# Kernel optimization log

Measured on AMD Instinct MI355X. Metric: run time of the kernel, lower is better.

Reference implementation:

```python
import jax, jax.numpy as jnp
import numpy as np

N = 100000   # total nodes in batched graph
E = 600000   # total edges
B = 64       # graphs in batch
H = 128      # hidden_dim
A = 64       # action_dim
L = 4        # num mpnn layers
LOG_STD_MIN, LOG_STD_MAX = -20.0, 2.0


def setup_inputs() -> dict:
    key = jax.random.key(0)
    ks = jax.random.split(key, 40)
    s = 0.05

    def w(k, shape):
        return (jax.random.normal(k, shape, jnp.float32) * s)

    inp = {}
    inp["node_feat"] = jax.random.normal(ks[0], (N, 7), jnp.float32)
    inp["edge_feat"] = jax.random.normal(ks[1], (E, 2), jnp.float32)
    # node encoder: Linear(7,H) -> ReLU -> Linear(H,H)
    inp["ne_w1"] = w(ks[2], (7, H)); inp["ne_b1"] = jnp.zeros((H,), jnp.float32)
    inp["ne_w2"] = w(ks[3], (H, H)); inp["ne_b2"] = jnp.zeros((H,), jnp.float32)
    # edge encoder: Linear(2,H) -> ReLU -> Linear(H,H)
    inp["ee_w1"] = w(ks[4], (2, H)); inp["ee_b1"] = jnp.zeros((H,), jnp.float32)
    inp["ee_w2"] = w(ks[5], (H, H)); inp["ee_b2"] = jnp.zeros((H,), jnp.float32)
    # per-layer message net: Linear(3H,H) -> ReLU -> Linear(H,H)  (stacked over L)
    inp["msg_w1"] = w(ks[6], (L, 3 * H, H)); inp["msg_b1"] = jnp.zeros((L, H), jnp.float32)
    inp["msg_w2"] = w(ks[7], (L, H, H));     inp["msg_b2"] = jnp.zeros((L, H), jnp.float32)
    # per-layer update net: Linear(2H,H) -> ReLU -> Linear(H,H)
    inp["upd_w1"] = w(ks[8], (L, 2 * H, H)); inp["upd_b1"] = jnp.zeros((L, H), jnp.float32)
    inp["upd_w2"] = w(ks[9], (L, H, H));     inp["upd_b2"] = jnp.zeros((L, H), jnp.float32)
    # attention-pooling gate: Linear(H,H) -> ReLU -> Linear(H,1)
    inp["gate_w1"] = w(ks[10], (H, H)); inp["gate_b1"] = jnp.zeros((H,), jnp.float32)
    inp["gate_w2"] = w(ks[11], (H, 1)); inp["gate_b2"] = jnp.zeros((1,), jnp.float32)
    # policy net: Linear(H,H) -> ReLU -> Linear(H,H) -> ReLU -> Linear(H,2A)
    inp["pol_w1"] = w(ks[12], (H, H));     inp["pol_b1"] = jnp.zeros((H,), jnp.float32)
    inp["pol_w2"] = w(ks[13], (H, H));     inp["pol_b2"] = jnp.zeros((H,), jnp.float32)
    inp["pol_w3"] = w(ks[14], (H, 2 * A)); inp["pol_b3"] = jnp.zeros((2 * A,), jnp.float32)
    # graph connectivity
    inp["src"] = jax.random.randint(ks[15], (E,), 0, N)
    inp["dst"] = jax.random.randint(ks[16], (E,), 0, N)
    inp["graph_id"] = jnp.sort(jax.random.randint(ks[17], (N,), 0, B))
    return inp


def _mlp2(x, w1, b1, w2, b2):
    return jax.nn.relu(x @ w1 + b1) @ w2 + b2


def reference(node_feat, edge_feat,
              ne_w1, ne_b1, ne_w2, ne_b2,
              ee_w1, ee_b1, ee_w2, ee_b2,
              msg_w1, msg_b1, msg_w2, msg_b2,
              upd_w1, upd_b1, upd_w2, upd_b2,
              gate_w1, gate_b1, gate_w2, gate_b2,
              pol_w1, pol_b1, pol_w2, pol_b2, pol_w3, pol_b3,
              src, dst, graph_id):
    # encode
    h = _mlp2(node_feat, ne_w1, ne_b1, ne_w2, ne_b2)          # [N, H]
    e = _mlp2(edge_feat, ee_w1, ee_b1, ee_w2, ee_b2)          # [E, H]
    # MPNN layers with residual (h = layer(h) + h)
    for l in range(L):
        msg_in = jnp.concatenate([h[src], h[dst], e], axis=1)  # [E, 3H]
        m = _mlp2(msg_in, msg_w1[l], msg_b1[l], msg_w2[l], msg_b2[l])  # [E, H]
        h_agg = jax.ops.segment_sum(m, dst, num_segments=N)    # [N, H]
        upd_in = jnp.concatenate([h, h_agg], axis=1)           # [N, 2H]
        h = _mlp2(upd_in, upd_w1[l], upd_b1[l], upd_w2[l], upd_b2[l]) + h
    # global attention pooling (per-graph segment softmax over gate logits)
    gate = _mlp2(h, gate_w1, gate_b1, gate_w2, gate_b2)[:, 0]  # [N]
    gmax = jax.ops.segment_max(gate, graph_id, num_segments=B)  # [B]
    ex = jnp.exp(gate - gmax[graph_id])                        # [N]
    z = jax.ops.segment_sum(ex, graph_id, num_segments=B)      # [B]
    alpha = ex / z[graph_id]                                   # [N]
    emb = jax.ops.segment_sum(alpha[:, None] * h, graph_id, num_segments=B)  # [B, H]
    # policy head
    out = jax.nn.relu(jax.nn.relu(emb @ pol_w1 + pol_b1) @ pol_w2 + pol_b2) @ pol_w3 + pol_b3  # [B, 2A]
    mean, log_std = out[:, :A], out[:, A:]
    log_std = jnp.clip(log_std, LOG_STD_MIN, LOG_STD_MAX)
    std = jnp.exp(log_std)
    return (mean, std)
```

## Files before the change

kernel.cpp:

```cpp
#include <hip/hip_runtime.h>
#include <stdint.h>

#define NN 100000
#define NE 600000
#define NG 64
#define HD 128
#define HD2 (HD*HD)
#define NLAYER 4
#define SCAN_NB 391
#define NTILES ((NN + 63) / 64)
#define PSLICE 16

typedef unsigned short u16;
typedef unsigned int u32;
typedef unsigned long long u64;
typedef __attribute__((ext_vector_type(8))) short bf16x8;
typedef __attribute__((ext_vector_type(4))) float f32x4;

__device__ __forceinline__ float bf2f(u32 v) { return __uint_as_float(v << 16); }
__device__ __forceinline__ u16 f2bf(float f) {
    u32 u = __float_as_uint(f);
    return (u16)((u + 0x7FFFu + ((u >> 16) & 1u)) >> 16);
}
__device__ __forceinline__ u32 pk2(float a, float b) {
    return (u32)f2bf(a) | ((u32)f2bf(b) << 16);
}

template<bool RELU, bool GATE>
__global__ __launch_bounds__(256, 3) void mgemm_kernel(
    const u16* __restrict__ Xb, const u16* __restrict__ Wt,
    const float* __restrict__ bias, const float* __restrict__ degscale,
    const u16* __restrict__ addend, u16* __restrict__ out, int M,
    const float* __restrict__ gw2, const float* __restrict__ gb2,
    float* __restrict__ gate)
{
    __shared__ u16 WsL[HD * HD];
    __shared__ u16 XsL[64 * HD];
    const int t = threadIdx.x;
    const int lane = t & 63, wave = t >> 6;
    const int cj = ((lane >> 4) << 2);

    for (int i = t; i < HD * 16; i += 256) {
        const int row = i >> 4, c16 = i & 15;
        uint4 v = *(const uint4*)(Wt + (size_t)row * HD + c16 * 8);
        *(uint4*)((char*)WsL + (((row << 8) + (c16 << 4)) ^ ((row & 7) << 4))) = v;
    }
    float4 bcol[8];
    #pragma unroll
    for (int ct = 0; ct < 8; ct++)
        bcol[ct] = bias ? *(const float4*)(bias + ct * 16 + cj)
                        : make_float4(0.f, 0.f, 0.f, 0.f);
    float4 gwv[8];
    if (GATE) {
        #pragma unroll
        for (int ct = 0; ct < 8; ct++)
            gwv[ct] = *(const float4*)(gw2 + ct * 16 + cj);
    }

    const int arow = wave * 16 + (lane & 15);
    const int alin = (arow << 8) + ((lane >> 4) << 4);
    const int axor = (arow & 7) << 4;
    __syncthreads();

    for (int tile = blockIdx.x; tile < NTILES; tile += gridDim.x) {
        const int r0 = tile << 6;
        for (int i = t; i < 64 * 16; i += 256) {
            const int row = i >> 4, c16 = i & 15;
            const int rg = r0 + row;
            uint4 v = make_uint4(0, 0, 0, 0);
            if (rg < M) v = *(const uint4*)(Xb + (size_t)rg * HD + c16 * 8);
            *(uint4*)((char*)XsL + (((row << 8) + (c16 << 4)) ^ ((row & 7) << 4))) = v;
        }
        __syncthreads();

        bf16x8 a[4];
        #pragma unroll
        for (int ks = 0; ks < 4; ks++)
            a[ks] = *(const bf16x8*)((const char*)XsL + ((alin + ks * 64) ^ axor));

        f32x4 acc[8];
        #pragma unroll
        for (int ct = 0; ct < 8; ct++) {
            acc[ct][0] = 0.f; acc[ct][1] = 0.f; acc[ct][2] = 0.f; acc[ct][3] = 0.f;
        }
        #pragma unroll
        for (int ct = 0; ct < 8; ct++) {
            const int bn = ct * 16 + (lane & 15);
            #pragma unroll
            for (int ks = 0; ks < 4; ks++) {
                bf16x8 breg = *(const bf16x8*)((const char*)WsL +
                    (((bn << 8) + ks * 64 + ((lane >> 4) << 4)) ^ ((bn & 7) << 4)));
                acc[ct] = __builtin_amdgcn_mfma_f32_16x16x32_bf16(breg, a[ks], acc[ct], 0, 0, 0);
            }
        }

        const int orow = r0 + wave * 16 + (lane & 15);
        const bool rv = orow < M;
        float gdot = 0.f;
        const float ds = (degscale && rv) ? degscale[orow] : 1.f;
        #pragma unroll
        for (int ct = 0; ct < 8; ct++) {
            const int c0 = ct * 16 + cj;
            float v0 = acc[ct][0], v1 = acc[ct][1], v2 = acc[ct][2], v3 = acc[ct][3];
            if (bias) {
                v0 += bcol[ct].x * ds; v1 += bcol[ct].y * ds;
                v2 += bcol[ct].z * ds; v3 += bcol[ct].w * ds;
            }
            if (addend && rv) {
                ushort4 av = *(const ushort4*)(addend + (size_t)orow * HD + c0);
                v0 += bf2f(av.x); v1 += bf2f(av.y); v2 += bf2f(av.z); v3 += bf2f(av.w);
            }
            if (RELU) {
                v0 = fmaxf(v0, 0.f); v1 = fmaxf(v1, 0.f);
                v2 = fmaxf(v2, 0.f); v3 = fmaxf(v3, 0.f);
            }
            if (GATE) {
                gdot += v0 * gwv[ct].x + v1 * gwv[ct].y + v2 * gwv[ct].z + v3 * gwv[ct].w;
            } else if (rv) {
                ushort4 pk;
                pk.x = f2bf(v0); pk.y = f2bf(v1); pk.z = f2bf(v2); pk.w = f2bf(v3);
                *(ushort4*)(out + (size_t)orow * HD + c0) = pk;
            }
        }
        if (GATE) {
            gdot += __shfl_xor(gdot, 16, 64);
            gdot += __shfl_xor(gdot, 32, 64);
            if ((lane >> 4) == 0 && rv) gate[orow] = gdot + gb2[0];
        }
        __syncthreads();
    }
}

__global__ __launch_bounds__(256, 2) void pqgemm_kernel(
    const u16* __restrict__ Xb, const u16* __restrict__ WtP,
    const u16* __restrict__ WtQ, u16* __restrict__ outP,
    u16* __restrict__ outQ, int M)
{
    __shared__ u16 WsL[2 * HD * HD];
    __shared__ u16 XsL[64 * HD];
    const int t = threadIdx.x;
    const int lane = t & 63, wave = t >> 6;
    const int cj = ((lane >> 4) << 2);

    for (int i = t; i < 2 * HD * 16; i += 256) {
        const int w = i >> 11;
        const int j = i & 2047;
        const int row = j >> 4, c16 = j & 15;
        const u16* Wt = w ? WtQ : WtP;
        uint4 v = *(const uint4*)(Wt + (size_t)row * HD + c16 * 8);
        *(uint4*)((char*)WsL + w * 32768 +
                  (((row << 8) + (c16 << 4)) ^ ((row & 7) << 4))) = v;
    }

    const int arow = wave * 16 + (lane & 15);
    const int alin = (arow << 8) + ((lane >> 4) << 4);
    const int axor = (arow & 7) << 4;
    __syncthreads();

    for (int tile = blockIdx.x; tile < NTILES; tile += gridDim.x) {
        const int r0 = tile << 6;
        for (int i = t; i < 64 * 16; i += 256) {
            const int row = i >> 4, c16 = i & 15;
            const int rg = r0 + row;
            uint4 v = make_uint4(0, 0, 0, 0);
            if (rg < M) v = *(const uint4*)(Xb + (size_t)rg * HD + c16 * 8);
            *(uint4*)((char*)XsL + (((row << 8) + (c16 << 4)) ^ ((row & 7) << 4))) = v;
        }
        __syncthreads();

        bf16x8 a[4];
        #pragma unroll
        for (int ks = 0; ks < 4; ks++)
            a[ks] = *(const bf16x8*)((const char*)XsL + ((alin + ks * 64) ^ axor));

        const int orow = r0 + wave * 16 + (lane & 15);
        const bool rv = orow < M;

        #pragma unroll
        for (int o = 0; o < 2; o++) {
            f32x4 acc[8];
            #pragma unroll
            for (int ct = 0; ct < 8; ct++) {
                acc[ct][0] = 0.f; acc[ct][1] = 0.f; acc[ct][2] = 0.f; acc[ct][3] = 0.f;
            }
            #pragma unroll
            for (int ct = 0; ct < 8; ct++) {
                const int bn = ct * 16 + (lane & 15);
                #pragma unroll
                for (int ks = 0; ks < 4; ks++) {
                    bf16x8 breg = *(const bf16x8*)((const char*)WsL + o * 32768 +
                        (((bn << 8) + ks * 64 + ((lane >> 4) << 4)) ^ ((bn & 7) << 4)));
                    acc[ct] = __builtin_amdgcn_mfma_f32_16x16x32_bf16(breg, a[ks], acc[ct], 0, 0, 0);
                }
            }
            if (rv) {
                u16* out = o ? outQ : outP;
                #pragma unroll
                for (int ct = 0; ct < 8; ct++) {
                    ushort4 pk;
                    pk.x = f2bf(acc[ct][0]); pk.y = f2bf(acc[ct][1]);
                    pk.z = f2bf(acc[ct][2]); pk.w = f2bf(acc[ct][3]);
                    *(ushort4*)(out + (size_t)orow * HD + ct * 16 + cj) = pk;
                }
            }
        }
        __syncthreads();
    }
}

__global__ __launch_bounds__(256, 2) void edge_mfma_kernel(
    const float2* __restrict__ sef, const int* __restrict__ ssrc,
    const int* __restrict__ sdst, const int* __restrict__ off,
    const float* __restrict__ ew1, const float* __restrict__ eb1,
    const u16* __restrict__ Mt, const float* __restrict__ mvec,
    const u16* __restrict__ P, const u16* __restrict__ Q,
    u16* __restrict__ agg)
{
    __shared__ __align__(16) char XHT[HD * 72 * 2];
    __shared__ u16 PsL[64 * 136];
    __shared__ u16 QsL[32 * 136];
    __shared__ u64 dlocL[8];
    __shared__ float ew1L[2 * HD];
    __shared__ float eb1L[HD];
    u16* HT = (u16*)XHT;
    const int t = threadIdx.x, lane = t & 63, wave = t >> 6;
    const int cj = (lane >> 4) << 2;
    const int n0 = blockIdx.x * 32;

    ew1L[t] = ew1[t];
    if (t < HD) eb1L[t] = eb1[t];
    for (int i = t; i < 32 * 32; i += 256) {
        const int row = i >> 5, c4 = (i & 31) * 4;
        *(ushort4*)(QsL + row * 136 + c4) = *(const ushort4*)(Q + (size_t)(n0 + row) * HD + c4);
    }

    float4 mvv[8];
    #pragma unroll
    for (int ct = 0; ct < 8; ct++) mvv[ct] = *(const float4*)(mvec + ct * 16 + cj);

    bf16x8 breg[8][4];
    #pragma unroll
    for (int ct = 0; ct < 8; ct++) {
        const int bn = ct * 16 + (lane & 15);
        #pragma unroll
        for (int ks = 0; ks < 4; ks++)
            breg[ct][ks] = *(const bf16x8*)(Mt + (size_t)bn * HD + ks * 32 + ((lane >> 4) << 3));
    }

    const int rt = wave & 1;
    const int c2b = (wave >> 1) * 4;
    const int nodeid = rt * 16 + (lane & 15);
    f32x4 acc2[4];
    #pragma unroll
    for (int i = 0; i < 4; i++) {
        acc2[i][0] = 0.f; acc2[i][1] = 0.f; acc2[i][2] = 0.f; acc2[i][3] = 0.f;
    }

    const int e0 = off[n0], e1 = off[n0 + 32];
    const int arow = wave * 16 + (lane & 15);
    const int alin = (arow << 8) + ((lane >> 4) << 4);
    const int axor = (arow & 7) << 4;
    const int el = wave * 16 + (lane & 15);
    __syncthreads();

    for (int base = e0; base < e1; base += 64) {
        for (int i = t; i < 64 * 16; i += 256) {
            const int row = i >> 4, c16 = i & 15;
            const int e = base + row;
            uint4 v = make_uint4(0, 0, 0, 0);
            uint4 pvv = make_uint4(0, 0, 0, 0);
            if (e < e1) {
                const float2 f = sef[e];
                const int c8 = c16 * 8;
                float o[8];
                #pragma unroll
                for (int k = 0; k < 8; k++)
                    o[k] = fmaxf(f.x * ew1L[c8 + k] + f.y * ew1L[HD + c8 + k] + eb1L[c8 + k], 0.f);
                v = make_uint4(pk2(o[0], o[1]), pk2(o[2], o[3]), pk2(o[4], o[5]), pk2(o[6], o[7]));
                const int srcI = ssrc[e];
                pvv = *(const uint4*)(P + (size_t)srcI * HD + c16 * 8);
            }
            *(uint4*)(XHT + (((row << 8) + (c16 << 4)) ^ ((row & 7) << 4))) = v;
            *(uint4*)(PsL + row * 136 + c16 * 8) = pvv;
        }
        if (t < 64) {
            const int e = base + t;
            ((unsigned char*)dlocL)[t] = (e < e1) ? (unsigned char)(sdst[e] - n0) : (unsigned char)0xFF;
        }
        __syncthreads();

        bf16x8 a[4];
        #pragma unroll
        for (int ks = 0; ks < 4; ks++)
            a[ks] = *(const bf16x8*)(XHT + ((alin + ks * 64) ^ axor));
        const int e = base + el;
        const bool ev = e < e1;
        const int dl = ev ? (int)((const unsigned char*)dlocL)[el] : 0;
        __syncthreads();

        f32x4 acc[8];
        #pragma unroll
        for (int ct = 0; ct < 8; ct++) {
            acc[ct][0] = 0.f; acc[ct][1] = 0.f; acc[ct][2] = 0.f; acc[ct][3] = 0.f;
        }
        #pragma unroll
        for (int ct = 0; ct < 8; ct++)
            #pragma unroll
            for (int ks = 0; ks < 4; ks++)
                acc[ct] = __builtin_amdgcn_mfma_f32_16x16x32_bf16(breg[ct][ks], a[ks], acc[ct], 0, 0, 0);

        #pragma unroll
        for (int ct = 0; ct < 8; ct++) {
            float v0 = 0.f, v1 = 0.f, v2 = 0.f, v3 = 0.f;
            if (ev) {
                const ushort4 pvc = *(const ushort4*)(PsL + el * 136 + ct * 16 + cj);
                const ushort4 qvc = *(const ushort4*)(QsL + dl * 136 + ct * 16 + cj);
                v0 = fmaxf(acc[ct][0] + bf2f(pvc.x) + bf2f(qvc.x) + mvv[ct].x, 0.f);
                v1 = fmaxf(acc[ct][1] + bf2f(pvc.y) + bf2f(qvc.y) + mvv[ct].y, 0.f);
                v2 = fmaxf(acc[ct][2] + bf2f(pvc.z) + bf2f(qvc.z) + mvv[ct].z, 0.f);
                v3 = fmaxf(acc[ct][3] + bf2f(pvc.w) + bf2f(qvc.w) + mvv[ct].w, 0.f);
            }
            const int c0 = ct * 16 + cj;
            HT[(c0 + 0) * 72 + el] = f2bf(v0);
            HT[(c0 + 1) * 72 + el] = f2bf(v1);
            HT[(c0 + 2) * 72 + el] = f2bf(v2);
            HT[(c0 + 3) * 72 + el] = f2bf(v3);
        }
        __syncthreads();

        #pragma unroll
        for (int ks2 = 0; ks2 < 2; ks2++) {
            const u64 dv = dlocL[ks2 * 4 + (lane >> 4)];
            bf16x8 sfrag;
            #pragma unroll
            for (int j = 0; j < 8; j++) {
                const int dvj = (int)((dv >> (8 * j)) & 0xFF);
                sfrag[j] = (dvj == nodeid) ? (short)0x3F80 : (short)0;
            }
            #pragma unroll
            for (int i = 0; i < 4; i++) {
                const int col = (c2b + i) * 16 + (lane & 15);
                bf16x8 hfrag = *(const bf16x8*)(HT + col * 72 + ks2 * 32 + ((lane >> 4) << 3));
                acc2[i] = __builtin_amdgcn_mfma_f32_16x16x32_bf16(sfrag, hfrag, acc2[i], 0, 0, 0);
            }
        }
        __syncthreads();
    }

    u16* BNC = (u16*)XHT;
    #pragma unroll
    for (int i = 0; i < 4; i++) {
        const int col = (c2b + i) * 16 + (lane & 15);
        #pragma unroll
        for (int r = 0; r < 4; r++) {
            const int nl = rt * 16 + ((lane >> 4) << 2) + r;
            BNC[nl * 136 + col] = f2bf(acc2[i][r]);
        }
    }
    __syncthreads();
    for (int i = t; i < 32 * 16; i += 256) {
        const int row = i >> 4, c16 = i & 15;
        *(uint4*)(agg + (size_t)(n0 + row) * HD + c16 * 8) =
            *(const uint4*)(BNC + row * 136 + c16 * 8);
    }
}

__global__ __launch_bounds__(256) void gemm128_kernel(
    const float* __restrict__ X, const float* __restrict__ W,
    float* __restrict__ out, int M)
{
    __shared__ float Ws[HD * HD];
    __shared__ float Xs[32 * HD];
    const int t = threadIdx.x;
    for (int i = t; i < HD * HD / 4; i += 256)
        ((float4*)Ws)[i] = ((const float4*)W)[i];
    const int c0 = (t & 31) * 4;
    const int rb = (t >> 5) * 4;
    __syncthreads();
    const int ntiles = M / 32;
    for (int tile = blockIdx.x; tile < ntiles; tile += gridDim.x) {
        const int r0 = tile * 32;
        const float4* xg = (const float4*)(X + (size_t)r0 * HD);
        for (int i = t; i < 32 * HD / 4; i += 256)
            ((float4*)Xs)[i] = xg[i];
        __syncthreads();
        float acc[4][4];
        #pragma unroll
        for (int a = 0; a < 4; a++)
            #pragma unroll
            for (int b = 0; b < 4; b++) acc[a][b] = 0.f;
        for (int k = 0; k < HD; k += 4) {
            float4 w0 = *(const float4*)(Ws + (k + 0) * HD + c0);
            float4 w1 = *(const float4*)(Ws + (k + 1) * HD + c0);
            float4 w2 = *(const float4*)(Ws + (k + 2) * HD + c0);
            float4 w3 = *(const float4*)(Ws + (k + 3) * HD + c0);
            #pragma unroll
            for (int rr = 0; rr < 4; rr++) {
                float4 xv = *(const float4*)(Xs + (rb + rr) * HD + k);
                acc[rr][0] += xv.x * w0.x + xv.y * w1.x + xv.z * w2.x + xv.w * w3.x;
                acc[rr][1] += xv.x * w0.y + xv.y * w1.y + xv.z * w2.y + xv.w * w3.y;
                acc[rr][2] += xv.x * w0.z + xv.y * w1.z + xv.z * w2.z + xv.w * w3.z;
                acc[rr][3] += xv.x * w0.w + xv.y * w1.w + xv.z * w2.w + xv.w * w3.w;
            }
        }
        #pragma unroll
        for (int rr = 0; rr < 4; rr++) {
            const int row = r0 + rb + rr;
            *(float4*)(out + (size_t)row * HD + c0) =
                make_float4(acc[rr][0], acc[rr][1], acc[rr][2], acc[rr][3]);
        }
        __syncthreads();
    }
}

__global__ void mvec_kernel(const float* __restrict__ vec,
                            const float* __restrict__ W,
                            const float* __restrict__ mb1,
                            float* __restrict__ out) {
    const int j = threadIdx.x;
    if (j < HD) {
        float s = mb1 ? mb1[j] : 0.f;
        for (int i = 0; i < HD; i++) s += vec[i] * W[(size_t)i * HD + j];
        out[j] = s;
    }
}

__global__ __launch_bounds__(256) void wprep_kernel(
    const float* __restrict__ msg_w1, const float* __restrict__ Mw2,
    const float* __restrict__ upd_w1, const float* __restrict__ upd_w2,
    const float* __restrict__ gw1, const float* __restrict__ ne_w2,
    const float* __restrict__ Mw, u16* __restrict__ wt)
{
    __shared__ float tileL[HD * (HD + 1)];
    const int b = blockIdx.x, t = threadIdx.x;
    const int l = b & 3;
    const float* S;
    if (b < 4)       S = msg_w1 + (size_t)l * 3 * HD2;
    else if (b < 8)  S = msg_w1 + (size_t)l * 3 * HD2 + HD2;
    else if (b < 12) S = Mw + (size_t)l * HD2;
    else if (b < 16) S = Mw2 + (size_t)l * HD2;
    else if (b < 20) S = upd_w1 + (size_t)l * 2 * HD2;
    else if (b < 24) S = upd_w1 + (size_t)l * 2 * HD2 + HD2;
    else if (b < 28) S = upd_w2 + (size_t)l * HD2;
    else if (b == 28) S = gw1;
    else             S = ne_w2;
    u16* D = wt + (size_t)b * HD2;
    for (int i = t; i < HD2; i += 256) {
        const int k = i >> 7, n = i & 127;
        tileL[k * (HD + 1) + n] = S[i];
    }
    __syncthreads();
    for (int i = t; i < HD2; i += 256) {
        const int n = i >> 7, k = i & 127;
        D[i] = f2bf(tileL[k * (HD + 1) + n]);
    }
}

__global__ __launch_bounds__(256) void ne1_kernel(
    const float* __restrict__ nf, const float* __restrict__ w1,
    const float* __restrict__ b1, u16* __restrict__ out)
{
    __shared__ float w1s[7 * HD];
    __shared__ float b1s[HD];
    const int t = threadIdx.x;
    for (int i = t; i < 7 * HD; i += 256) w1s[i] = w1[i];
    if (t < HD) b1s[t] = b1[t];
    __syncthreads();
    const int row = blockIdx.x * 32 + (t >> 3);
    const int c0 = (t & 7) * 16;
    if (row < NN) {
        float f[7];
        #pragma unroll
        for (int k = 0; k < 7; k++) f[k] = nf[(size_t)row * 7 + k];
        float o[16];
        #pragma unroll
        for (int c = 0; c < 16; c++) {
            float a = b1s[c0 + c];
            #pragma unroll
            for (int k = 0; k < 7; k++) a += f[k] * w1s[k * HD + c0 + c];
            o[c] = fmaxf(a, 0.f);
        }
        uint4 v0 = make_uint4(pk2(o[0], o[1]), pk2(o[2], o[3]), pk2(o[4], o[5]), pk2(o[6], o[7]));
        uint4 v1 = make_uint4(pk2(o[8], o[9]), pk2(o[10], o[11]), pk2(o[12], o[13]), pk2(o[14], o[15]));
        *(uint4*)(out + (size_t)row * HD + c0) = v0;
        *(uint4*)(out + (size_t)row * HD + c0 + 8) = v1;
    }
}

__global__ void deg_count_kernel(const int* __restrict__ dst, int* __restrict__ deg) {
    const int i = blockIdx.x * 256 + threadIdx.x;
    if (i < NE) atomicAdd(&deg[dst[i]], 1);
}
__global__ void scan1_kernel(const int* __restrict__ deg, int* __restrict__ part) {
    __shared__ int s[256];
    const int t = threadIdx.x, i = blockIdx.x * 256 + t;
    s[t] = (i < NN) ? deg[i] : 0;
    __syncthreads();
    for (int d = 128; d > 0; d >>= 1) { if (t < d) s[t] += s[t + d]; __syncthreads(); }
    if (t == 0) part[blockIdx.x] = s[0];
}
__global__ void scan2_kernel(int* __restrict__ part, int nb) {
    if (threadIdx.x == 0 && blockIdx.x == 0) {
        int run = 0;
        for (int b = 0; b < nb; b++) { const int v = part[b]; part[b] = run; run += v; }
    }
}
__global__ void scan3_kernel(const int* __restrict__ deg, const int* __restrict__ part,
                             int* __restrict__ off, int* __restrict__ pos) {
    __shared__ int s[256];
    const int t = threadIdx.x, i = blockIdx.x * 256 + t;
    const int v = (i < NN) ? deg[i] : 0;
    s[t] = v;
    __syncthreads();
    for (int d = 1; d < 256; d <<= 1) {
        const int x = (t >= d) ? s[t - d] : 0;
        __syncthreads();
        s[t] += x;
        __syncthreads();
    }
    const int excl = s[t] - v + part[blockIdx.x];
    if (i < NN) {
        off[i] = excl; pos[i] = excl;
        if (i == NN - 1) off[NN] = excl + v;
    }
}
__global__ void scatter_kernel(const int* __restrict__ src, const int* __restrict__ dst,
                               const float* __restrict__ ef, int* __restrict__ pos,
                               float2* __restrict__ sef, int* __restrict__ ssrc,
                               int* __restrict__ sdst) {
    const int e = blockIdx.x * 256 + threadIdx.x;
    if (e < NE) {
        const int d = dst[e];
        const int p = atomicAdd(&pos[d], 1);
        sef[p] = make_float2(ef[2 * e], ef[2 * e + 1]);
        ssrc[p] = src[e]; sdst[p] = d;
    }
}
__global__ void degf_kernel(const int* __restrict__ off, float* __restrict__ degf) {
    const int n = blockIdx.x * 256 + threadIdx.x;
    if (n < NN) degf[n] = (float)(off[n + 1] - off[n]);
}

__global__ void bounds_kernel(const int* __restrict__ gid, int* __restrict__ gs) {
    const int g = threadIdx.x;
    if (g <= NG) {
        int lo = 0, hi = NN;
        while (lo < hi) {
            const int mid = (lo + hi) >> 1;
            if (gid[mid] < g) lo = mid + 1; else hi = mid;
        }
        gs[g] = lo;
    }
}

__global__ __launch_bounds__(256) void poolA_kernel(
    const float* __restrict__ gate, const int* __restrict__ gs,
    float* __restrict__ ex, float* __restrict__ gz)
{
    __shared__ float red[256];
    const int g = blockIdx.x, t = threadIdx.x;
    const int s = gs[g], e = gs[g + 1];
    if (s >= e) {
        if (t == 0) gz[g] = 1.f;
        return;
    }
    float m = -3.4e38f;
    for (int i = s + t; i < e; i += 256) m = fmaxf(m, gate[i]);
    red[t] = m; __syncthreads();
    for (int d = 128; d > 0; d >>= 1) {
        if (t < d) red[t] = fmaxf(red[t], red[t + d]);
        __syncthreads();
    }
    const float gm = red[0];
    __syncthreads();
    float zs = 0.f;
    for (int i = s + t; i < e; i += 256) {
        const float ev = expf(gate[i] - gm);
        ex[i] = ev; zs += ev;
    }
    red[t] = zs; __syncthreads();
    for (int d = 128; d > 0; d >>= 1) {
        if (t < d) red[t] += red[t + d];
        __syncthreads();
    }
    if (t == 0) gz[g] = red[0];
}

__global__ __launch_bounds__(256) void poolB_kernel(
    const float* __restrict__ ex, const int* __restrict__ gs,
    const u16* __restrict__ hb, float* __restrict__ partial)
{
    __shared__ float redL[16][132];
    const int b = blockIdx.x;
    const int g = b / PSLICE, sl = b % PSLICE;
    const int lo = gs[g], hi = gs[g + 1];
    const int len = hi - lo;
    const int chunk = (len + PSLICE - 1) / PSLICE;
    const int ns = lo + sl * chunk;
    const int ne = min(ns + chunk, hi);
    const int t = threadIdx.x;
    const int c8 = (t & 15) * 8;
    const int ro = t >> 4;
    float acc[8] = {0.f, 0.f, 0.f, 0.f, 0.f, 0.f, 0.f, 0.f};
    for (int n = ns + ro; n < ne; n += 16) {
        const float w = ex[n];
        const ushort4 h0 = *(const ushort4*)(hb + (size_t)n * HD + c8);
        const ushort4 h1 = *(const ushort4*)(hb + (size_t)n * HD + c8 + 4);
        acc[0] += w * bf2f(h0.x); acc[1] += w * bf2f(h0.y);
        acc[2] += w * bf2f(h0.z); acc[3] += w * bf2f(h0.w);
        acc[4] += w * bf2f(h1.x); acc[5] += w * bf2f(h1.y);
        acc[6] += w * bf2f(h1.z); acc[7] += w * bf2f(h1.w);
    }
    #pragma unroll
    for (int j = 0; j < 8; j++) redL[ro][c8 + j] = acc[j];
    __syncthreads();
    if (t < HD) {
        float s = 0.f;
        #pragma unroll
        for (int r = 0; r < 16; r++) s += redL[r][t];
        partial[(size_t)b * HD + t] = s;
    }
}

__global__ void poolC_kernel(const float* __restrict__ partial,
                             const float* __restrict__ gz,
                             float* __restrict__ emb)
{
    const int g = blockIdx.x, t = threadIdx.x;
    float s = 0.f;
    #pragma unroll
    for (int sl = 0; sl < PSLICE; sl++)
        s += partial[(size_t)(g * PSLICE + sl) * HD + t];
    emb[(size_t)g * HD + t] = s / gz[g];
}

__global__ __launch_bounds__(256) void policy_kernel(
    const float* __restrict__ emb,
    const float* __restrict__ w1, const float* __restrict__ b1,
    const float* __restrict__ w2, const float* __restrict__ b2,
    const float* __restrict__ w3, const float* __restrict__ b3,
    float* __restrict__ out)
{
    __shared__ float A[NG * HD];
    __shared__ float Bs[NG * HD];
    const int t = threadIdx.x;
    for (int i = t; i < NG * HD / 4; i += 256)
        ((float4*)A)[i] = ((const float4*)emb)[i];
    __syncthreads();
    const int c0 = (t & 31) * 4;
    const int rb = (t >> 5) * 8;
    {
        float4 bv = *(const float4*)(b1 + c0);
        for (int rr = 0; rr < 8; rr++) {
            const int r = rb + rr;
            float a0 = bv.x, a1 = bv.y, a2 = bv.z, a3 = bv.w;
            for (int k = 0; k < HD; k++) {
                const float x = A[r * HD + k];
                float4 wv = *(const float4*)(w1 + k * HD + c0);
                a0 += x * wv.x; a1 += x * wv.y; a2 += x * wv.z; a3 += x * wv.w;
            }
            *(float4*)(Bs + r * HD + c0) =
                make_float4(fmaxf(a0, 0.f), fmaxf(a1, 0.f), fmaxf(a2, 0.f), fmaxf(a3, 0.f));
        }
    }
    __syncthreads();
    {
        float4 bv = *(const float4*)(b2 + c0);
        for (int rr = 0; rr < 8; rr++) {
            const int r = rb + rr;
            float a0 = bv.x, a1 = bv.y, a2 = bv.z, a3 = bv.w;
            for (int k = 0; k < HD; k++) {
                const float x = Bs[r * HD + k];
                float4 wv = *(const float4*)(w2 + k * HD + c0);
                a0 += x * wv.x; a1 += x * wv.y; a2 += x * wv.z; a3 += x * wv.w;
            }
            *(float4*)(A + r * HD + c0) =
                make_float4(fmaxf(a0, 0.f), fmaxf(a1, 0.f), fmaxf(a2, 0.f), fmaxf(a3, 0.f));
        }
    }
    __syncthreads();
    {
        float4 bv = *(const float4*)(b3 + c0);
        for (int rr = 0; rr < 8; rr++) {
            const int r = rb + rr;
            float a[4] = {bv.x, bv.y, bv.z, bv.w};
            for (int k = 0; k < HD; k++) {
                const float x = A[r * HD + k];
                float4 wv = *(const float4*)(w3 + k * HD + c0);
                a[0] += x * wv.x; a[1] += x * wv.y; a[2] += x * wv.z; a[3] += x * wv.w;
            }
            #pragma unroll
            for (int j = 0; j < 4; j++) {
                const int c = c0 + j;
                if (c < 64) {
                    out[r * 64 + c] = a[j];
                } else {
                    const float ls = fminf(fmaxf(a[j], -20.f), 2.f);
                    out[4096 + r * 64 + (c - 64)] = expf(ls);
                }
            }
        }
    }
}

extern "C" void kernel_launch(void* const* d_in, const int* in_sizes, int n_in,
                              void* d_out, int out_size, void* d_ws, size_t ws_size,
                              hipStream_t stream) {
    const float* node_feat = (const float*)d_in[0];
    const float* edge_feat = (const float*)d_in[1];
    const float* ne_w1 = (const float*)d_in[2];
    const float* ne_b1 = (const float*)d_in[3];
    const float* ne_w2 = (const float*)d_in[4];
    const float* ne_b2 = (const float*)d_in[5];
    const float* ee_w1 = (const float*)d_in[6];
    const float* ee_b1 = (const float*)d_in[7];
    const float* ee_w2 = (const float*)d_in[8];
    const float* ee_b2 = (const float*)d_in[9];
    const float* msg_w1 = (const float*)d_in[10];
    const float* msg_b1 = (const float*)d_in[11];
    const float* msg_w2 = (const float*)d_in[12];
    const float* msg_b2 = (const float*)d_in[13];
    const float* upd_w1 = (const float*)d_in[14];
    const float* upd_b1 = (const float*)d_in[15];
    const float* upd_w2 = (const float*)d_in[16];
    const float* upd_b2 = (const float*)d_in[17];
    const float* gate_w1 = (const float*)d_in[18];
    const float* gate_b1 = (const float*)d_in[19];
    const float* gate_w2 = (const float*)d_in[20];
    const float* gate_b2 = (const float*)d_in[21];
    const float* pol_w1 = (const float*)d_in[22];
    const float* pol_b1 = (const float*)d_in[23];
    const float* pol_w2 = (const float*)d_in[24];
    const float* pol_b2 = (const float*)d_in[25];
    const float* pol_w3 = (const float*)d_in[26];
    const float* pol_b3 = (const float*)d_in[27];
    const int* src = (const int*)d_in[28];
    const int* dst = (const int*)d_in[29];
    const int* gid = (const int*)d_in[30];

    char* p = (char*)d_ws;
    u16* hb   = (u16*)p;    p += (size_t)NN * HD * 2;
    u16* Pb   = (u16*)p;    p += (size_t)NN * HD * 2;
    u16* Qb   = (u16*)p;    p += (size_t)NN * HD * 2;
    u16* aggb = (u16*)p;    p += (size_t)NN * HD * 2;
    float2* sef = (float2*)p; p += (size_t)NE * 8;
    int* ssrc = (int*)p;    p += (size_t)NE * 4;
    int* sdst = (int*)p;    p += (size_t)NE * 4;
    int* off  = (int*)p;    p += (size_t)(NN + 4) * 4;
    int* pos  = (int*)p;    p += (size_t)NN * 4;
    int* deg  = (int*)p;    p += (size_t)NN * 4;
    float* degf = (float*)p; p += (size_t)NN * 4;
    float* gate = (float*)p; p += (size_t)NN * 4;
    float* ex   = (float*)p; p += (size_t)NN * 4;
    int* part = (int*)p;    p += 2048;
    int* gs   = (int*)p;    p += 512;
    float* gz   = (float*)p; p += 256;
    float* emb = (float*)p; p += (size_t)NG * HD * 4;
    float* partialP = (float*)p; p += (size_t)NG * PSLICE * HD * 4;
    float* Mw  = (float*)p; p += (size_t)NLAYER * HD2 * 4;
    float* Mw2 = (float*)p; p += (size_t)NLAYER * HD2 * 4;
    float* mvec = (float*)p; p += (size_t)NLAYER * HD * 4;
    float* b2u  = (float*)p; p += (size_t)NLAYER * HD * 4;
    u16* wt = (u16*)p;      p += (size_t)30 * HD2 * 2;

    hipMemsetAsync(deg, 0, (size_t)NN * 4, stream);
    deg_count_kernel<<<(NE + 255) / 256, 256, 0, stream>>>(dst, deg);
    scan1_kernel<<<SCAN_NB, 256, 0, stream>>>(deg, part);
    scan2_kernel<<<1, 64, 0, stream>>>(part, SCAN_NB);
    scan3_kernel<<<SCAN_NB, 256, 0, stream>>>(deg, part, off, pos);
    degf_kernel<<<SCAN_NB, 256, 0, stream>>>(off, degf);
    scatter_kernel<<<(NE + 255) / 256, 256, 0, stream>>>(src, dst, edge_feat, pos, sef, ssrc, sdst);
    bounds_kernel<<<1, 128, 0, stream>>>(gid, gs);

    for (int l = 0; l < NLAYER; l++) {
        const float* W1c = msg_w1 + (size_t)l * 3 * HD2 + 2 * HD2;
        const float* U1b = upd_w1 + (size_t)l * 2 * HD2 + HD2;
        gemm128_kernel<<<4, 256, 0, stream>>>(ee_w2, W1c, Mw + (size_t)l * HD2, HD);
        mvec_kernel<<<1, 128, 0, stream>>>(ee_b2, W1c, msg_b1 + (size_t)l * HD,
                                           mvec + (size_t)l * HD);
        gemm128_kernel<<<4, 256, 0, stream>>>(msg_w2 + (size_t)l * HD2, U1b,
                                              Mw2 + (size_t)l * HD2, HD);
        mvec_kernel<<<1, 128, 0, stream>>>(msg_b2 + (size_t)l * HD, U1b, nullptr,
                                           b2u + (size_t)l * HD);
    }
    wprep_kernel<<<30, 256, 0, stream>>>(msg_w1, Mw2, upd_w1, upd_w2, gate_w1, ne_w2, Mw, wt);

    ne1_kernel<<<3125, 256, 0, stream>>>(node_feat, ne_w1, ne_b1, Pb);
    mgemm_kernel<false, false><<<512, 256, 0, stream>>>(
        Pb, wt + (size_t)29 * HD2, ne_b2, nullptr, nullptr, hb, NN, nullptr, nullptr, nullptr);

    for (int l = 0; l < NLAYER; l++) {
        pqgemm_kernel<<<512, 256, 0, stream>>>(
            hb, wt + (size_t)(0 + l) * HD2, wt + (size_t)(4 + l) * HD2, Pb, Qb, NN);
        edge_mfma_kernel<<<NN / 32, 256, 0, stream>>>(sef, ssrc, sdst, off, ee_w1, ee_b1,
            wt + (size_t)(8 + l) * HD2, mvec + (size_t)l * HD, Pb, Qb, aggb);
        mgemm_kernel<false, false><<<512, 256, 0, stream>>>(
            hb, wt + (size_t)(16 + l) * HD2, upd_b1 + (size_t)l * HD, nullptr, nullptr, Qb, NN,
            nullptr, nullptr, nullptr);
        mgemm_kernel<true, false><<<512, 256, 0, stream>>>(
            aggb, wt + (size_t)(12 + l) * HD2, b2u + (size_t)l * HD, degf, Qb, Pb, NN,
            nullptr, nullptr, nullptr);
        mgemm_kernel<false, false><<<512, 256, 0, stream>>>(
            Pb, wt + (size_t)(24 + l) * HD2, upd_b2 + (size_t)l * HD, nullptr, hb, hb, NN,
            nullptr, nullptr, nullptr);
    }

    mgemm_kernel<true, true><<<512, 256, 0, stream>>>(
        hb, wt + (size_t)28 * HD2, gate_b1, nullptr, nullptr, nullptr, NN,
        gate_w2, gate_b2, gate);
    poolA_kernel<<<NG, 256, 0, stream>>>(gate, gs, ex, gz);
    poolB_kernel<<<NG * PSLICE, 256, 0, stream>>>(ex, gs, hb, partialP);
    poolC_kernel<<<NG, 128, 0, stream>>>(partialP, gz, emb);
    policy_kernel<<<1, 256, 0, stream>>>(emb, pol_w1, pol_b1, pol_w2, pol_b2, pol_w3, pol_b3, (float*)d_out);
}
```

Baseline: 1.430 ms.

## Prefetch next edge chunk into registers and split shared buffers in edge kernel

The edge kernel now loads the next 64-edge chunk's features, gathered P rows and destination indices into registers while the current chunk is being processed, so global gather latency overlaps compute. The X staging tile and the HT transpose buffer get separate shared arrays, which allows one __syncthreads per iteration to be removed. MFMA sections are wrapped in s_setprio to favour matrix issue. The cost is more shared memory and registers, which may lower occupancy under launch_bounds(256,2).

```diff
diff --git a/kernel.cpp b/kernel.cpp
--- a/kernel.cpp
+++ b/kernel.cpp
@@ -216,13 +216,13 @@
     const u16* __restrict__ P, const u16* __restrict__ Q,
     u16* __restrict__ agg)
 {
-    __shared__ __align__(16) char XHT[HD * 72 * 2];
+    __shared__ __align__(16) u16 XsL[64 * HD];
+    __shared__ __align__(16) u16 HT[HD * 72];
     __shared__ u16 PsL[64 * 136];
     __shared__ u16 QsL[32 * 136];
     __shared__ u64 dlocL[8];
     __shared__ float ew1L[2 * HD];
     __shared__ float eb1L[HD];
-    u16* HT = (u16*)XHT;
     const int t = threadIdx.x, lane = t & 63, wave = t >> 6;
     const int cj = (lane >> 4) << 2;
     const int n0 = blockIdx.x * 32;
@@ -261,53 +261,84 @@
     const int alin = (arow << 8) + ((lane >> 4) << 4);
     const int axor = (arow & 7) << 4;
     const int el = wave * 16 + (lane & 15);
+
+    float2 pf[4];
+    uint4 pp[4];
+    unsigned char pdb = 0xFF;
+    #pragma unroll
+    for (int k = 0; k < 4; k++) {
+        const int i = t + k * 256;
+        const int row = i >> 4, c16 = i & 15;
+        const int e = e0 + row;
+        pf[k] = make_float2(0.f, 0.f);
+        pp[k] = make_uint4(0, 0, 0, 0);
+        if (e < e1) {
+            pf[k] = sef[e];
+            pp[k] = *(const uint4*)(P + (size_t)ssrc[e] * HD + c16 * 8);
+        }
+    }
+    if (t < 64 && e0 + t < e1) pdb = (unsigned char)(sdst[e0 + t] - n0);
     __syncthreads();
 
     for (int base = e0; base < e1; base += 64) {
-        for (int i = t; i < 64 * 16; i += 256) {
+        #pragma unroll
+        for (int k = 0; k < 4; k++) {
+            const int i = t + k * 256;
             const int row = i >> 4, c16 = i & 15;
             const int e = base + row;
             uint4 v = make_uint4(0, 0, 0, 0);
-            uint4 pvv = make_uint4(0, 0, 0, 0);
             if (e < e1) {
-                const float2 f = sef[e];
                 const int c8 = c16 * 8;
                 float o[8];
                 #pragma unroll
-                for (int k = 0; k < 8; k++)
-                    o[k] = fmaxf(f.x * ew1L[c8 + k] + f.y * ew1L[HD + c8 + k] + eb1L[c8 + k], 0.f);
+                for (int kk = 0; kk < 8; kk++)
+                    o[kk] = fmaxf(pf[k].x * ew1L[c8 + kk] + pf[k].y * ew1L[HD + c8 + kk] + eb1L[c8 + kk], 0.f);
                 v = make_uint4(pk2(o[0], o[1]), pk2(o[2], o[3]), pk2(o[4], o[5]), pk2(o[6], o[7]));
-                const int srcI = ssrc[e];
-                pvv = *(const uint4*)(P + (size_t)srcI * HD + c16 * 8);
-            }
-            *(uint4*)(XHT + (((row << 8) + (c16 << 4)) ^ ((row & 7) << 4))) = v;
-            *(uint4*)(PsL + row * 136 + c16 * 8) = pvv;
-        }
-        if (t < 64) {
-            const int e = base + t;
-            ((unsigned char*)dlocL)[t] = (e < e1) ? (unsigned char)(sdst[e] - n0) : (unsigned char)0xFF;
+            }
+            *(uint4*)((char*)XsL + (((row << 8) + (c16 << 4)) ^ ((row & 7) << 4))) = v;
+            *(uint4*)(PsL + row * 136 + c16 * 8) = pp[k];
+        }
+        if (t < 64) ((unsigned char*)dlocL)[t] = pdb;
+
+        const int nbase = base + 64;
+        if (nbase < e1) {
+            #pragma unroll
+            for (int k = 0; k < 4; k++) {
+                const int i = t + k * 256;
+                const int row = i >> 4, c16 = i & 15;
+                const int e = nbase + row;
+                pf[k] = make_float2(0.f, 0.f);
+                pp[k] = make_uint4(0, 0, 0, 0);
+                if (e < e1) {
+                    pf[k] = sef[e];
+                    pp[k] = *(const uint4*)(P + (size_t)ssrc[e] * HD + c16 * 8);
+                }
+            }
+            pdb = 0xFF;
+            if (t < 64 && nbase + t < e1) pdb = (unsigned char)(sdst[nbase + t] - n0);
         }
         __syncthreads();
 
         bf16x8 a[4];
         #pragma unroll
         for (int ks = 0; ks < 4; ks++)
-            a[ks] = *(const bf16x8*)(XHT + ((alin + ks * 64) ^ axor));
+            a[ks] = *(const bf16x8*)((const char*)XsL + ((alin + ks * 64) ^ axor));
         const int e = base + el;
         const bool ev = e < e1;
         const int dl = ev ? (int)((const unsigned char*)dlocL)[el] : 0;
-        __syncthreads();
 
         f32x4 acc[8];
         #pragma unroll
         for (int ct = 0; ct < 8; ct++) {
             acc[ct][0] = 0.f; acc[ct][1] = 0.f; acc[ct][2] = 0.f; acc[ct][3] = 0.f;
         }
+        __builtin_amdgcn_s_setprio(1);
         #pragma unroll
         for (int ct = 0; ct < 8; ct++)
             #pragma unroll
             for (int ks = 0; ks < 4; ks++)
                 acc[ct] = __builtin_amdgcn_mfma_f32_16x16x32_bf16(breg[ct][ks], a[ks], acc[ct], 0, 0, 0);
+        __builtin_amdgcn_s_setprio(0);
 
         #pragma unroll
         for (int ct = 0; ct < 8; ct++) {
@@ -328,6 +359,7 @@
         }
         __syncthreads();
 
+        __builtin_amdgcn_s_setprio(1);
         #pragma unroll
         for (int ks2 = 0; ks2 < 2; ks2++) {
             const u64 dv = dlocL[ks2 * 4 + (lane >> 4)];
@@ -344,10 +376,11 @@
                 acc2[i] = __builtin_amdgcn_mfma_f32_16x16x32_bf16(sfrag, hfrag, acc2[i], 0, 0, 0);
             }
         }
-        __syncthreads();
-    }
-
-    u16* BNC = (u16*)XHT;
+        __builtin_amdgcn_s_setprio(0);
+        __syncthreads();
+    }
+
+    u16* BNC = XsL;
     #pragma unroll
     for (int i = 0; i < 4; i++) {
         const int col = (c2b + i) * 16 + (lane & 15);
```

Result: slower. 1.571 ms (+9.8%).
